# Kernel tuning notes

Measured on AMD Instinct MI355X. Metric: run time of the kernel, lower is better.

Reference implementation:

```python
import jax, jax.numpy as jnp
import numpy as np

TIMESCALE = 10.0   # NeuralODE init kwarg
N_MAX = 48         # static upper bound on number of constant-size Dopri5 steps
B, D, H = 8192, 128, 128


def _mlp(y, W1, b1, W2, b2):
    # autonomous dynamics f(x): tanh MLP, applied along last dim
    return jnp.tanh(y @ W1 + b1) @ W2 + b2


def _dopri5_step(y, dt, f):
    # classic Dormand-Prince 5(4) tableau; autonomous f, so c_i unused
    k1 = f(y)
    k2 = f(y + dt * (1.0 / 5.0 * k1))
    k3 = f(y + dt * (3.0 / 40.0 * k1 + 9.0 / 40.0 * k2))
    k4 = f(y + dt * (44.0 / 45.0 * k1 - 56.0 / 15.0 * k2 + 32.0 / 9.0 * k3))
    k5 = f(y + dt * (19372.0 / 6561.0 * k1 - 25360.0 / 2187.0 * k2
                     + 64448.0 / 6561.0 * k3 - 212.0 / 729.0 * k4))
    k6 = f(y + dt * (9017.0 / 3168.0 * k1 - 355.0 / 33.0 * k2
                     + 46732.0 / 5247.0 * k3 + 49.0 / 176.0 * k4
                     - 5103.0 / 18656.0 * k5))
    return y + dt * (35.0 / 384.0 * k1 + 500.0 / 1113.0 * k3
                     + 125.0 / 192.0 * k4 - 2187.0 / 6784.0 * k5
                     + 11.0 / 84.0 * k6)


def _initial_step_size(y0, f0, f, order=4, rtol=1.4e-8, atol=1.4e-8):
    # faithful port of NeuralODE.initial_step_size (Hairer heuristic)
    scale = atol + jnp.abs(y0) * rtol
    d0 = jnp.linalg.norm(y0 / scale)
    d1 = jnp.linalg.norm(f0 / scale)
    h0 = jnp.where((d0 < 1e-5) | (d1 < 1e-5), 1e-6, 0.01 * d0 / d1)
    y1 = y0 + h0 * f0
    f1 = f(y1)
    d2 = jnp.linalg.norm((f1 - f0) / scale) / h0
    h1 = jnp.where((d1 <= 1e-15) & (d2 <= 1e-15),
                   jnp.maximum(1e-6, h0 * 1e-3),
                   (0.01 / (d1 + d2)) ** (1.0 / (order + 1.0)))
    return jnp.minimum(100.0 * h0, h1)


def setup_inputs() -> dict:
    key = jax.random.key(0)
    k0, k1, k2 = jax.random.split(key, 3)
    x = jax.random.normal(k0, (B, D), jnp.float32)
    W1 = jax.random.normal(k1, (D, H), jnp.float32) * (1.0 / D ** 0.5)
    b1 = jnp.zeros((H,), jnp.float32)
    W2 = jax.random.normal(k2, (H, D), jnp.float32) * (1.0 / H ** 0.5)
    b2 = jnp.zeros((D,), jnp.float32)
    t = jnp.ones((1,), jnp.float32)
    return {"t": t, "x": x, "W1": W1, "b1": b1, "W2": W2, "b2": b2}


def reference(t, x, W1, b1, W2, b2):
    f = lambda y: _mlp(y, W1, b1, W2, b2)
    # dt0 from the first state row, exactly as the original (x[0, :])
    dt0 = _initial_step_size(x[0], f(x[0]), f)
    T = t[0] / TIMESCALE  # linspace(0, t/timescale, 2) -> ts = [0, T]

    # diffrax default ConstantStepSize: fixed-dt Dopri5 until t reaches T.
    # Static-length scan with dt clamped to the remaining interval; once
    # t == T, dt == 0 and the step is skipped via lax.cond.
    step = jax.checkpoint(
        lambda y, dt: jax.lax.cond(dt > 0.0,
                                   lambda a: _dopri5_step(a, dt, f),
                                   lambda a: a, y))

    def body(carry, _):
        tt, y = carry
        dt = jnp.clip(T - tt, 0.0, dt0)
        return (tt + dt, step(y, dt)), None

    (_, yT), _ = jax.lax.scan(body, (jnp.zeros((), jnp.float32), x), None,
                              length=N_MAX)
    # SaveAt(ts=[0, T]) -> ys has leading axis n_samples=2
    return jnp.stack([x, yT])
```

## Files before the change

### kernel.cpp

```cpp
#include <hip/hip_runtime.h>


typedef __attribute__((ext_vector_type(8))) short short8;
typedef __attribute__((ext_vector_type(4))) float f32x4;

#define SL 136

__device__ __forceinline__ short f2bf(float f) {
  union { float f; unsigned u; } v; v.f = f;
  return (short)((v.u + 0x8000u) >> 16);
}

__device__ __forceinline__ unsigned pack2bf(float lo, float hi) {
  union { float f; unsigned u; } a, b; a.f = lo; b.f = hi;
  return __builtin_amdgcn_perm(b.u + 0x8000u, a.u + 0x8000u, 0x07060302u);
}

__device__ __forceinline__ float fast_tanh(float x) {
  float e = __expf(2.0f * x);
  return 1.0f - __fdividef(2.0f, e + 1.0f);
}

__global__ __launch_bounds__(256, 2)
void node_kernel(const float* __restrict__ tptr, const float* __restrict__ x,
                 const float* __restrict__ W1, const float* __restrict__ b1,
                 const float* __restrict__ W2, const float* __restrict__ b2,
                 float* __restrict__ out) {
  const int tid  = threadIdx.x;
  const int lane = tid & 63;
  const int w    = tid >> 6;
  const int q    = lane >> 4;
  const int mL   = lane & 15;
  const int blockRow = blockIdx.x * 16;

  __shared__ short Yb[16 * SL];
  __shared__ short Tb[16 * SL];
  __shared__ float sred[256];
  __shared__ float spart[2][128];
  __shared__ float srowY[128], srowH[128], srowF[128], srowY2[128], srowF2[128], sscale[128];

  short8 w1t[2][4], w2t[2][4];
  f32x4 b1v[2], b2v[2];
#pragma unroll
  for (int s = 0; s < 2; ++s) {
    const int ft = (2 * w + s) * 16;
#pragma unroll
    for (int r = 0; r < 4; ++r) { b1v[s][r] = b1[ft + q * 4 + r]; b2v[s][r] = b2[ft + q * 4 + r]; }
#pragma unroll
    for (int kt = 0; kt < 4; ++kt) {
      short8 v1, v2;
#pragma unroll
      for (int j = 0; j < 8; ++j) {
        const int k = kt * 32 + q * 8 + j;
        v1[j] = f2bf(W1[k * 128 + ft + mL]);
        v2[j] = f2bf(W2[k * 128 + ft + mL]);
      }
      w1t[s][kt] = v1; w2t[s][kt] = v2;
    }
  }

  auto block_sum = [&](float v) -> float {
    sred[tid] = v;
    __syncthreads();
    if (tid < 64) {
      float s = sred[tid] + sred[tid + 64] + sred[tid + 128] + sred[tid + 192];
#pragma unroll
      for (int o = 32; o > 0; o >>= 1) s += __shfl_down(s, o, 64);
      if (tid == 0) sred[0] = s;
    }
    __syncthreads();
    float r = sred[0];
    __syncthreads();
    return r;
  };

  auto mlp_layer = [&](const float* vin, const float* Wg, const float* bg,
                       float* vout, bool dotanh) {
    const int col = tid & 127, part = tid >> 7;
    float s = 0.f;
    const float* wp = Wg + (part * 64) * 128 + col;
#pragma unroll 8
    for (int j = 0; j < 64; ++j) s += vin[part * 64 + j] * wp[j * 128];
    spart[part][col] = s;
    __syncthreads();
    if (tid < 128) {
      float a = bg[tid] + spart[0][tid] + spart[1][tid];
      vout[tid] = dotanh ? fast_tanh(a) : a;
    }
    __syncthreads();
  };

  if (tid < 128) srowY[tid] = x[tid];
  __syncthreads();
  mlp_layer(srowY, W1, b1, srowH, true);
  mlp_layer(srowH, W2, b2, srowF, false);
  float t0 = 0.f, t1 = 0.f;
  if (tid < 128) {
    float sc = 1.4e-8f + fabsf(srowY[tid]) * 1.4e-8f;
    sscale[tid] = sc;
    float a = srowY[tid] / sc; t0 = a * a;
    float bq = srowF[tid] / sc; t1 = bq * bq;
  }
  float d0 = sqrtf(block_sum(t0));
  float d1 = sqrtf(block_sum(t1));
  float h0 = (d0 < 1e-5f || d1 < 1e-5f) ? 1e-6f : 0.01f * d0 / d1;
  if (tid < 128) srowY2[tid] = srowY[tid] + h0 * srowF[tid];
  __syncthreads();
  mlp_layer(srowY2, W1, b1, srowH, true);
  mlp_layer(srowH, W2, b2, srowF2, false);
  float t2 = 0.f;
  if (tid < 128) { float a = (srowF2[tid] - srowF[tid]) / sscale[tid]; t2 = a * a; }
  float d2 = sqrtf(block_sum(t2)) / h0;
  float h1 = (d1 <= 1e-15f && d2 <= 1e-15f) ? fmaxf(1e-6f, h0 * 1e-3f)
                                            : powf(0.01f / (d1 + d2), 0.2f);
  const float dt0v = fminf(100.f * h0, h1);

  f32x4 yr[2];
#pragma unroll
  for (int s = 0; s < 2; ++s)
    yr[s] = *(const f32x4*)&x[(blockRow + mL) * 128 + (2 * w + s) * 16 + q * 4];

  const int rowOff = mL * SL;
  const int wrOff0 = rowOff + (2 * w) * 16 + q * 4;
  const int wrOff1 = wrOff0 + 16;
  const int rdOff  = rowOff + q * 8;

  auto evalF = [&](const f32x4* yin, f32x4* kout) {
    *(uint2*)&Yb[wrOff0] = uint2{pack2bf(yin[0][0], yin[0][1]), pack2bf(yin[0][2], yin[0][3])};
    *(uint2*)&Yb[wrOff1] = uint2{pack2bf(yin[1][0], yin[1][1]), pack2bf(yin[1][2], yin[1][3])};
    __syncthreads();
    f32x4 acc0 = b1v[0], acc1 = b1v[1];
    short8 rb0 = *(const short8*)&Yb[rdOff];
    short8 rb1 = *(const short8*)&Yb[rdOff + 32];
    short8 rb2 = *(const short8*)&Yb[rdOff + 64];
    short8 rb3 = *(const short8*)&Yb[rdOff + 96];
    acc0 = __builtin_amdgcn_mfma_f32_16x16x32_bf16(w1t[0][0], rb0, acc0, 0, 0, 0);
    acc1 = __builtin_amdgcn_mfma_f32_16x16x32_bf16(w1t[1][0], rb0, acc1, 0, 0, 0);
    acc0 = __builtin_amdgcn_mfma_f32_16x16x32_bf16(w1t[0][1], rb1, acc0, 0, 0, 0);
    acc1 = __builtin_amdgcn_mfma_f32_16x16x32_bf16(w1t[1][1], rb1, acc1, 0, 0, 0);
    acc0 = __builtin_amdgcn_mfma_f32_16x16x32_bf16(w1t[0][2], rb2, acc0, 0, 0, 0);
    acc1 = __builtin_amdgcn_mfma_f32_16x16x32_bf16(w1t[1][2], rb2, acc1, 0, 0, 0);
    acc0 = __builtin_amdgcn_mfma_f32_16x16x32_bf16(w1t[0][3], rb3, acc0, 0, 0, 0);
    acc1 = __builtin_amdgcn_mfma_f32_16x16x32_bf16(w1t[1][3], rb3, acc1, 0, 0, 0);
    *(uint2*)&Tb[wrOff0] = uint2{pack2bf(fast_tanh(acc0[0]), fast_tanh(acc0[1])),
                                 pack2bf(fast_tanh(acc0[2]), fast_tanh(acc0[3]))};
    *(uint2*)&Tb[wrOff1] = uint2{pack2bf(fast_tanh(acc1[0]), fast_tanh(acc1[1])),
                                 pack2bf(fast_tanh(acc1[2]), fast_tanh(acc1[3]))};
    __syncthreads();
    f32x4 accF0 = b2v[0], accF1 = b2v[1];
    short8 tb0 = *(const short8*)&Tb[rdOff];
    short8 tb1 = *(const short8*)&Tb[rdOff + 32];
    short8 tb2 = *(const short8*)&Tb[rdOff + 64];
    short8 tb3 = *(const short8*)&Tb[rdOff + 96];
    accF0 = __builtin_amdgcn_mfma_f32_16x16x32_bf16(w2t[0][0], tb0, accF0, 0, 0, 0);
    accF1 = __builtin_amdgcn_mfma_f32_16x16x32_bf16(w2t[1][0], tb0, accF1, 0, 0, 0);
    accF0 = __builtin_amdgcn_mfma_f32_16x16x32_bf16(w2t[0][1], tb1, accF0, 0, 0, 0);
    accF1 = __builtin_amdgcn_mfma_f32_16x16x32_bf16(w2t[1][1], tb1, accF1, 0, 0, 0);
    accF0 = __builtin_amdgcn_mfma_f32_16x16x32_bf16(w2t[0][2], tb2, accF0, 0, 0, 0);
    accF1 = __builtin_amdgcn_mfma_f32_16x16x32_bf16(w2t[1][2], tb2, accF1, 0, 0, 0);
    accF0 = __builtin_amdgcn_mfma_f32_16x16x32_bf16(w2t[0][3], tb3, accF0, 0, 0, 0);
    accF1 = __builtin_amdgcn_mfma_f32_16x16x32_bf16(w2t[1][3], tb3, accF1, 0, 0, 0);
    kout[0] = accF0; kout[1] = accF1;
  };

  const float T = tptr[0] / 10.0f;
  float tt = 0.f;
  f32x4 k1[2], k2[2], k3[2], k4[2], k5[2], k6[2], yv[2];

#pragma unroll 1
  for (int it = 0; it < 48; ++it) {
    float dt = fminf(fmaxf(T - tt, 0.f), dt0v);
    if (dt > 0.f) {
      evalF(yr, k1);
#pragma unroll
      for (int s = 0; s < 2; ++s) yv[s] = yr[s] + dt * (0.2f * k1[s]);
      evalF(yv, k2);
#pragma unroll
      for (int s = 0; s < 2; ++s) yv[s] = yr[s] + dt * (0.075f * k1[s] + 0.225f * k2[s]);
      evalF(yv, k3);
#pragma unroll
      for (int s = 0; s < 2; ++s)
        yv[s] = yr[s] + dt * (0.9777777777777777f * k1[s] - 3.7333333333333334f * k2[s]
                            + 3.5555555555555554f * k3[s]);
      evalF(yv, k4);
#pragma unroll
      for (int s = 0; s < 2; ++s)
        yv[s] = yr[s] + dt * (2.9525986892242035f * k1[s] - 11.595793324188385f * k2[s]
                            + 9.822892851699436f * k3[s] - 0.2908093278463649f * k4[s]);
      evalF(yv, k5);
#pragma unroll
      for (int s = 0; s < 2; ++s)
        yv[s] = yr[s] + dt * (2.8462752525252526f * k1[s] - 10.757575757575758f * k2[s]
                            + 8.906422717743473f * k3[s] + 0.2784090909090909f * k4[s]
                            - 0.27351165254237287f * k5[s]);
      evalF(yv, k6);
#pragma unroll
      for (int s = 0; s < 2; ++s)
        yr[s] = yr[s] + dt * (0.0911458333333333f * k1[s] + 0.449236298292902f * k3[s]
                            + 0.6510416666666666f * k4[s] - 0.32237617924528303f * k5[s]
                            + 0.13095238095238096f * k6[s]);
    }
    tt += dt;
  }

  {
    const float4* x4 = (const float4*)(x + blockRow * 128);
    float4* o4 = (float4*)(out + blockRow * 128);
#pragma unroll
    for (int i = 0; i < 2; ++i) o4[tid + 256 * i] = x4[tid + 256 * i];
    float* oy = out + 8192 * 128;
#pragma unroll
    for (int s = 0; s < 2; ++s)
      *(f32x4*)&oy[(blockRow + mL) * 128 + (2 * w + s) * 16 + q * 4] = yr[s];
  }
}

extern "C" void kernel_launch(void* const* d_in, const int* in_sizes, int n_in,
                              void* d_out, int out_size, void* d_ws, size_t ws_size,
                              hipStream_t stream) {
  const float* t  = (const float*)d_in[0];
  const float* x  = (const float*)d_in[1];
  const float* W1 = (const float*)d_in[2];
  const float* b1 = (const float*)d_in[3];
  const float* W2 = (const float*)d_in[4];
  const float* b2 = (const float*)d_in[5];
  float* out = (float*)d_out;
  node_kernel<<<dim3(512), dim3(256), 0, stream>>>(t, x, W1, b1, W2, b2, out);
}
```

Measured before the change: 172.7 us.

## Use 512-thread blocks with 8 waves each owning one feature tile over two row tiles

Each block now handles 32 rows with 8 waves, and each wave owns a single 16-column feature tile applied to two 16-row tiles. This halves the per-thread weight fragments held in registers, which lowers register pressure, and it halves the number of blocks, so the scalar initial-step-size computation is repeated half as often. The cost is that block-wide barriers now synchronise 8 waves instead of 4, and only 256 blocks cover the GPU's compute units.

```diff
diff --git a/kernel.cpp b/kernel.cpp
--- a/kernel.cpp
+++ b/kernel.cpp
@@ -21,7 +21,7 @@
   return 1.0f - __fdividef(2.0f, e + 1.0f);
 }
 
-__global__ __launch_bounds__(256, 2)
+__global__ __launch_bounds__(512, 2)
 void node_kernel(const float* __restrict__ tptr, const float* __restrict__ x,
                  const float* __restrict__ W1, const float* __restrict__ b1,
                  const float* __restrict__ W2, const float* __restrict__ b2,
@@ -31,39 +31,38 @@
   const int w    = tid >> 6;
   const int q    = lane >> 4;
   const int mL   = lane & 15;
-  const int blockRow = blockIdx.x * 16;
-
-  __shared__ short Yb[16 * SL];
-  __shared__ short Tb[16 * SL];
-  __shared__ float sred[256];
-  __shared__ float spart[2][128];
+  const int ft   = w * 16;
+  const int blockRow = blockIdx.x * 32;
+
+  __shared__ short YbA[16 * SL], YbB[16 * SL];
+  __shared__ short TbA[16 * SL], TbB[16 * SL];
+  __shared__ float sred[512];
+  __shared__ float spart[4][128];
   __shared__ float srowY[128], srowH[128], srowF[128], srowY2[128], srowF2[128], sscale[128];
 
-  short8 w1t[2][4], w2t[2][4];
-  f32x4 b1v[2], b2v[2];
-#pragma unroll
-  for (int s = 0; s < 2; ++s) {
-    const int ft = (2 * w + s) * 16;
-#pragma unroll
-    for (int r = 0; r < 4; ++r) { b1v[s][r] = b1[ft + q * 4 + r]; b2v[s][r] = b2[ft + q * 4 + r]; }
-#pragma unroll
-    for (int kt = 0; kt < 4; ++kt) {
-      short8 v1, v2;
-#pragma unroll
-      for (int j = 0; j < 8; ++j) {
-        const int k = kt * 32 + q * 8 + j;
-        v1[j] = f2bf(W1[k * 128 + ft + mL]);
-        v2[j] = f2bf(W2[k * 128 + ft + mL]);
-      }
-      w1t[s][kt] = v1; w2t[s][kt] = v2;
-    }
+  short8 w1t[4], w2t[4];
+  f32x4 b1v, b2v;
+#pragma unroll
+  for (int r = 0; r < 4; ++r) { b1v[r] = b1[ft + q * 4 + r]; b2v[r] = b2[ft + q * 4 + r]; }
+#pragma unroll
+  for (int kt = 0; kt < 4; ++kt) {
+    short8 v1, v2;
+#pragma unroll
+    for (int j = 0; j < 8; ++j) {
+      const int k = kt * 32 + q * 8 + j;
+      v1[j] = f2bf(W1[k * 128 + ft + mL]);
+      v2[j] = f2bf(W2[k * 128 + ft + mL]);
+    }
+    w1t[kt] = v1; w2t[kt] = v2;
   }
 
   auto block_sum = [&](float v) -> float {
     sred[tid] = v;
     __syncthreads();
     if (tid < 64) {
-      float s = sred[tid] + sred[tid + 64] + sred[tid + 128] + sred[tid + 192];
+      float s = 0.f;
+#pragma unroll
+      for (int i = 0; i < 8; ++i) s += sred[tid + 64 * i];
 #pragma unroll
       for (int o = 32; o > 0; o >>= 1) s += __shfl_down(s, o, 64);
       if (tid == 0) sred[0] = s;
@@ -78,13 +77,13 @@
                        float* vout, bool dotanh) {
     const int col = tid & 127, part = tid >> 7;
     float s = 0.f;
-    const float* wp = Wg + (part * 64) * 128 + col;
+    const float* wp = Wg + (part * 32) * 128 + col;
 #pragma unroll 8
-    for (int j = 0; j < 64; ++j) s += vin[part * 64 + j] * wp[j * 128];
+    for (int j = 0; j < 32; ++j) s += vin[part * 32 + j] * wp[j * 128];
     spart[part][col] = s;
     __syncthreads();
     if (tid < 128) {
-      float a = bg[tid] + spart[0][tid] + spart[1][tid];
+      float a = bg[tid] + spart[0][tid] + spart[1][tid] + spart[2][tid] + spart[3][tid];
       vout[tid] = dotanh ? fast_tanh(a) : a;
     }
     __syncthreads();
@@ -118,48 +117,44 @@
   f32x4 yr[2];
 #pragma unroll
   for (int s = 0; s < 2; ++s)
-    yr[s] = *(const f32x4*)&x[(blockRow + mL) * 128 + (2 * w + s) * 16 + q * 4];
-
-  const int rowOff = mL * SL;
-  const int wrOff0 = rowOff + (2 * w) * 16 + q * 4;
-  const int wrOff1 = wrOff0 + 16;
-  const int rdOff  = rowOff + q * 8;
-
-  auto evalF = [&](const f32x4* yin, f32x4* kout) {
-    *(uint2*)&Yb[wrOff0] = uint2{pack2bf(yin[0][0], yin[0][1]), pack2bf(yin[0][2], yin[0][3])};
-    *(uint2*)&Yb[wrOff1] = uint2{pack2bf(yin[1][0], yin[1][1]), pack2bf(yin[1][2], yin[1][3])};
-    __syncthreads();
-    f32x4 acc0 = b1v[0], acc1 = b1v[1];
-    short8 rb0 = *(const short8*)&Yb[rdOff];
-    short8 rb1 = *(const short8*)&Yb[rdOff + 32];
-    short8 rb2 = *(const short8*)&Yb[rdOff + 64];
-    short8 rb3 = *(const short8*)&Yb[rdOff + 96];
-    acc0 = __builtin_amdgcn_mfma_f32_16x16x32_bf16(w1t[0][0], rb0, acc0, 0, 0, 0);
-    acc1 = __builtin_amdgcn_mfma_f32_16x16x32_bf16(w1t[1][0], rb0, acc1, 0, 0, 0);
-    acc0 = __builtin_amdgcn_mfma_f32_16x16x32_bf16(w1t[0][1], rb1, acc0, 0, 0, 0);
-    acc1 = __builtin_amdgcn_mfma_f32_16x16x32_bf16(w1t[1][1], rb1, acc1, 0, 0, 0);
-    acc0 = __builtin_amdgcn_mfma_f32_16x16x32_bf16(w1t[0][2], rb2, acc0, 0, 0, 0);
-    acc1 = __builtin_amdgcn_mfma_f32_16x16x32_bf16(w1t[1][2], rb2, acc1, 0, 0, 0);
-    acc0 = __builtin_amdgcn_mfma_f32_16x16x32_bf16(w1t[0][3], rb3, acc0, 0, 0, 0);
-    acc1 = __builtin_amdgcn_mfma_f32_16x16x32_bf16(w1t[1][3], rb3, acc1, 0, 0, 0);
-    *(uint2*)&Tb[wrOff0] = uint2{pack2bf(fast_tanh(acc0[0]), fast_tanh(acc0[1])),
+    yr[s] = *(const f32x4*)&x[(blockRow + s * 16 + mL) * 128 + ft + q * 4];
+
+  const int wrOff = mL * SL + ft + q * 4;
+  const int rdOff = mL * SL + q * 8;
+
+  auto evalF2 = [&](const f32x4* yin, f32x4* kout) {
+    *(uint2*)&YbA[wrOff] = uint2{pack2bf(yin[0][0], yin[0][1]), pack2bf(yin[0][2], yin[0][3])};
+    *(uint2*)&YbB[wrOff] = uint2{pack2bf(yin[1][0], yin[1][1]), pack2bf(yin[1][2], yin[1][3])};
+    __syncthreads();
+    short8 rA[4], rB[4];
+#pragma unroll
+    for (int kt = 0; kt < 4; ++kt) {
+      rA[kt] = *(const short8*)&YbA[rdOff + kt * 32];
+      rB[kt] = *(const short8*)&YbB[rdOff + kt * 32];
+    }
+    f32x4 acc0 = b1v, acc1 = b1v;
+#pragma unroll
+    for (int kt = 0; kt < 4; ++kt) {
+      acc0 = __builtin_amdgcn_mfma_f32_16x16x32_bf16(w1t[kt], rA[kt], acc0, 0, 0, 0);
+      acc1 = __builtin_amdgcn_mfma_f32_16x16x32_bf16(w1t[kt], rB[kt], acc1, 0, 0, 0);
+    }
+    *(uint2*)&TbA[wrOff] = uint2{pack2bf(fast_tanh(acc0[0]), fast_tanh(acc0[1])),
                                  pack2bf(fast_tanh(acc0[2]), fast_tanh(acc0[3]))};
-    *(uint2*)&Tb[wrOff1] = uint2{pack2bf(fast_tanh(acc1[0]), fast_tanh(acc1[1])),
+    *(uint2*)&TbB[wrOff] = uint2{pack2bf(fast_tanh(acc1[0]), fast_tanh(acc1[1])),
                                  pack2bf(fast_tanh(acc1[2]), fast_tanh(acc1[3]))};
     __syncthreads();
-    f32x4 accF0 = b2v[0], accF1 = b2v[1];
-    short8 tb0 = *(const short8*)&Tb[rdOff];
-    short8 tb1 = *(const short8*)&Tb[rdOff + 32];
-    short8 tb2 = *(const short8*)&Tb[rdOff + 64];
-    short8 tb3 = *(const short8*)&Tb[rdOff + 96];
-    accF0 = __builtin_amdgcn_mfma_f32_16x16x32_bf16(w2t[0][0], tb0, accF0, 0, 0, 0);
-    accF1 = __builtin_amdgcn_mfma_f32_16x16x32_bf16(w2t[1][0], tb0, accF1, 0, 0, 0);
-    accF0 = __builtin_amdgcn_mfma_f32_16x16x32_bf16(w2t[0][1], tb1, accF0, 0, 0, 0);
-    accF1 = __builtin_amdgcn_mfma_f32_16x16x32_bf16(w2t[1][1], tb1, accF1, 0, 0, 0);
-    accF0 = __builtin_amdgcn_mfma_f32_16x16x32_bf16(w2t[0][2], tb2, accF0, 0, 0, 0);
-    accF1 = __builtin_amdgcn_mfma_f32_16x16x32_bf16(w2t[1][2], tb2, accF1, 0, 0, 0);
-    accF0 = __builtin_amdgcn_mfma_f32_16x16x32_bf16(w2t[0][3], tb3, accF0, 0, 0, 0);
-    accF1 = __builtin_amdgcn_mfma_f32_16x16x32_bf16(w2t[1][3], tb3, accF1, 0, 0, 0);
+    short8 tA[4], tB[4];
+#pragma unroll
+    for (int kt = 0; kt < 4; ++kt) {
+      tA[kt] = *(const short8*)&TbA[rdOff + kt * 32];
+      tB[kt] = *(const short8*)&TbB[rdOff + kt * 32];
+    }
+    f32x4 accF0 = b2v, accF1 = b2v;
+#pragma unroll
+    for (int kt = 0; kt < 4; ++kt) {
+      accF0 = __builtin_amdgcn_mfma_f32_16x16x32_bf16(w2t[kt], tA[kt], accF0, 0, 0, 0);
+      accF1 = __builtin_amdgcn_mfma_f32_16x16x32_bf16(w2t[kt], tB[kt], accF1, 0, 0, 0);
+    }
     kout[0] = accF0; kout[1] = accF1;
   };
 
@@ -171,29 +166,29 @@
   for (int it = 0; it < 48; ++it) {
     float dt = fminf(fmaxf(T - tt, 0.f), dt0v);
     if (dt > 0.f) {
-      evalF(yr, k1);
+      evalF2(yr, k1);
 #pragma unroll
       for (int s = 0; s < 2; ++s) yv[s] = yr[s] + dt * (0.2f * k1[s]);
-      evalF(yv, k2);
+      evalF2(yv, k2);
 #pragma unroll
       for (int s = 0; s < 2; ++s) yv[s] = yr[s] + dt * (0.075f * k1[s] + 0.225f * k2[s]);
-      evalF(yv, k3);
+      evalF2(yv, k3);
 #pragma unroll
       for (int s = 0; s < 2; ++s)
         yv[s] = yr[s] + dt * (0.9777777777777777f * k1[s] - 3.7333333333333334f * k2[s]
                             + 3.5555555555555554f * k3[s]);
-      evalF(yv, k4);
+      evalF2(yv, k4);
 #pragma unroll
       for (int s = 0; s < 2; ++s)
         yv[s] = yr[s] + dt * (2.9525986892242035f * k1[s] - 11.595793324188385f * k2[s]
                             + 9.822892851699436f * k3[s] - 0.2908093278463649f * k4[s]);
-      evalF(yv, k5);
+      evalF2(yv, k5);
 #pragma unroll
       for (int s = 0; s < 2; ++s)
         yv[s] = yr[s] + dt * (2.8462752525252526f * k1[s] - 10.757575757575758f * k2[s]
                             + 8.906422717743473f * k3[s] + 0.2784090909090909f * k4[s]
                             - 0.27351165254237287f * k5[s]);
-      evalF(yv, k6);
+      evalF2(yv, k6);
 #pragma unroll
       for (int s = 0; s < 2; ++s)
         yr[s] = yr[s] + dt * (0.0911458333333333f * k1[s] + 0.449236298292902f * k3[s]
@@ -207,11 +202,11 @@
     const float4* x4 = (const float4*)(x + blockRow * 128);
     float4* o4 = (float4*)(out + blockRow * 128);
 #pragma unroll
-    for (int i = 0; i < 2; ++i) o4[tid + 256 * i] = x4[tid + 256 * i];
+    for (int i = 0; i < 2; ++i) o4[tid + 512 * i] = x4[tid + 512 * i];
     float* oy = out + 8192 * 128;
 #pragma unroll
     for (int s = 0; s < 2; ++s)
-      *(f32x4*)&oy[(blockRow + mL) * 128 + (2 * w + s) * 16 + q * 4] = yr[s];
+      *(f32x4*)&oy[(blockRow + s * 16 + mL) * 128 + ft + q * 4] = yr[s];
   }
 }
 
@@ -225,5 +220,5 @@
   const float* W2 = (const float*)d_in[4];
   const float* b2 = (const float*)d_in[5];
   float* out = (float*)d_out;
-  node_kernel<<<dim3(512), dim3(256), 0, stream>>>(t, x, W1, b1, W2, b2, out);
-}
+  node_kernel<<<dim3(256), dim3(512), 0, stream>>>(t, x, W1, b1, W2, b2, out);
+}
```

Result: slower. 185.5 us (+7.4%).
